# Performance work log

Measured on AMD Instinct MI355X. Metric: run time of the kernel, lower is better.

## Reference

```python
import jax, jax.numpy as jnp
import numpy as np

EMBED_DIM = 768
HEAD_DIM = 64
BATCH = 8
SEQ = 4096


def setup_inputs() -> dict:
    key = jax.random.key(0)
    k_x, k_q, k_k, k_v = jax.random.split(key, 4)
    input_ids = jax.random.normal(k_x, (BATCH, SEQ, EMBED_DIM), dtype=jnp.float32)
    # nn.Linear(embed, head, bias=False): weight shape [head, embed]; y = x @ W.T
    scale = 1.0 / np.sqrt(EMBED_DIM)
    Wq = jax.random.normal(k_q, (HEAD_DIM, EMBED_DIM), dtype=jnp.float32) * scale
    Wk = jax.random.normal(k_k, (HEAD_DIM, EMBED_DIM), dtype=jnp.float32) * scale
    Wv = jax.random.normal(k_v, (HEAD_DIM, EMBED_DIM), dtype=jnp.float32) * scale
    return {"input_ids": input_ids, "Wq": Wq, "Wk": Wk, "Wv": Wv}


def reference(input_ids, Wq, Wk, Wv):
    # Projections. NOTE: the original module (faithfully reproduced) computes
    # v with q_net, so Wv is unused in the forward math.
    q = jnp.einsum('bse,he->bsh', input_ids, Wq)  # [B,S,H]
    k = jnp.einsum('bse,he->bsh', input_ids, Wk)  # [B,S,H]
    v = jnp.einsum('bse,he->bsh', input_ids, Wq)  # bug in source: uses q_net
    seq_len = q.shape[1]
    # Non-standard scaling: divide by sqrt(seq_len), not sqrt(head_dim)
    scores = jnp.einsum('bqh,bkh->bqk', q, k) / jnp.sqrt(jnp.float32(seq_len))
    # Non-standard softmax axis: over the query axis (dim=1)
    attn_weights = jax.nn.softmax(scores, axis=1)  # [B,Sq,Sk]
    return jnp.einsum('bqk,bkh->bqh', attn_weights, v)
```

## Files before the change

### kernel.cpp

```cpp
#include <hip/hip_runtime.h>
#include <hip/hip_bf16.h>
#include <cstdint>


#define BATCH 8
#define SEQ   4096
#define EMB   768
#define HD    64
#define NROW  (BATCH*SEQ)

#define QSCALE 0.1803368801111201f
#define KSCALE 0.125f
#define CSCALE 5.545177444479562f

typedef float  f32x4  __attribute__((ext_vector_type(4)));
typedef float  f32x16 __attribute__((ext_vector_type(16)));
typedef __bf16 bf16x8 __attribute__((ext_vector_type(8)));
typedef unsigned short u16x8_t __attribute__((ext_vector_type(8)));
typedef unsigned int   u32x4_t __attribute__((ext_vector_type(4)));

__device__ __forceinline__ f32x4 mfma16(bf16x8 a, bf16x8 b, f32x4 c) {
  return __builtin_amdgcn_mfma_f32_16x16x32_bf16(a, b, c, 0, 0, 0);
}
__device__ __forceinline__ f32x16 mfma32(bf16x8 a, bf16x8 b, f32x16 c) {
  return __builtin_amdgcn_mfma_f32_32x32x16_bf16(a, b, c, 0, 0, 0);
}
__device__ __forceinline__ unsigned short f2b(float f) {
  __bf16 h = (__bf16)f;
  return __builtin_bit_cast(unsigned short, h);
}
__device__ __forceinline__ float b2f(unsigned short u) {
  unsigned int x = ((unsigned int)u) << 16;
  return __builtin_bit_cast(float, x);
}
__device__ __forceinline__ unsigned short f2h(float f) {
  _Float16 h = (_Float16)f;
  return __builtin_bit_cast(unsigned short, h);
}
__device__ __forceinline__ float h2f(unsigned short u) {
  return (float)__builtin_bit_cast(_Float16, u);
}
__device__ __forceinline__ bf16x8 ldsA(const unsigned short* p) {
  return __builtin_bit_cast(bf16x8, *(const u16x8_t*)p);
}
__device__ __forceinline__ bf16x8 ldg8(const unsigned short* p) {
  return __builtin_bit_cast(bf16x8, *(const u16x8_t*)p);
}
__device__ __forceinline__ float expf2(float x) {
  float r; asm("v_exp_f32 %0, %1" : "=v"(r) : "v"(x)); return r;
}
__device__ __forceinline__ unsigned cvtpk(float lo, float hi) {
  unsigned r; asm("v_cvt_pk_bf16_f32 %0, %1, %2" : "=v"(r) : "v"(lo), "v"(hi)); return r;
}
__device__ __forceinline__ void plane32swap(unsigned &a, unsigned &b) {
  asm volatile("v_permlane32_swap_b32 %0, %1" : "+v"(a), "+v"(b));
}
__device__ __forceinline__ void glld16(const void* g, void* l) {
  __builtin_amdgcn_global_load_lds(
      (const __attribute__((address_space(1))) void*)g,
      (__attribute__((address_space(3))) void*)l, 16, 0, 0);
}
__device__ __forceinline__ int sidx(int r, int h) {
  return r * 64 + (h ^ ((r & 7) << 3));
}

__global__ __launch_bounds__(256) void wcvt_kernel(
    const float* __restrict__ Wq, const float* __restrict__ Wk,
    unsigned short* __restrict__ Wb) {
  int ci = blockIdx.x * 256 + threadIdx.x;
  int r = ci / 96, c8 = ci % 96;
  const float* src = (r < 64 ? Wq + (size_t)r * EMB : Wk + (size_t)(r - 64) * EMB) + c8 * 8;
  float4 a = *(const float4*)src, d = *(const float4*)(src + 4);
  u16x8_t o;
  o[0]=f2b(a.x); o[1]=f2b(a.y); o[2]=f2b(a.z); o[3]=f2b(a.w);
  o[4]=f2b(d.x); o[5]=f2b(d.y); o[6]=f2b(d.z); o[7]=f2b(d.w);
  *(u16x8_t*)(Wb + (size_t)ci * 8) = o;
}

__global__ __launch_bounds__(256) void proj_kernel(
    const float* __restrict__ X, const unsigned short* __restrict__ Wb,
    unsigned short* __restrict__ Qb, unsigned short* __restrict__ Kb) {
  __shared__ unsigned short Ws[2][8192];
  const int t = threadIdx.x, lane = t & 63, w = t >> 6;
  const int c = lane & 15, g = lane >> 4;
  const int row0 = blockIdx.x * 64;
  f32x4 acc[8];
#pragma unroll
  for (int f = 0; f < 8; ++f) { acc[f][0]=0.f; acc[f][1]=0.f; acc[f][2]=0.f; acc[f][3]=0.f; }

  auto STAGE = [&](int ec, int bb) {
#pragma unroll
    for (int i = 0; i < 4; ++i) {
      int rr = w + 4 * i;
      int ci = rr * 64 + lane;
      int r = ci >> 3, cL = ci & 7;
      glld16(Wb + (size_t)r * EMB + ec * 64 + (cL ^ (r & 7)) * 8, (void*)&Ws[bb][rr * 512]);
    }
  };
  STAGE(0, 0);
  __syncthreads();
  for (int ec = 0; ec < 12; ++ec) {
    if (ec < 11) STAGE(ec + 1, (ec + 1) & 1);
    bf16x8 Af[2];
#pragma unroll
    for (int es = 0; es < 2; ++es) {
      const float* xp = X + (size_t)(row0 + 16 * w + c) * EMB + ec * 64 + es * 32 + 8 * g;
      float4 v0 = *(const float4*)xp, v1 = *(const float4*)(xp + 4);
      u16x8_t tmp;
      tmp[0]=f2b(v0.x); tmp[1]=f2b(v0.y); tmp[2]=f2b(v0.z); tmp[3]=f2b(v0.w);
      tmp[4]=f2b(v1.x); tmp[5]=f2b(v1.y); tmp[6]=f2b(v1.z); tmp[7]=f2b(v1.w);
      Af[es] = __builtin_bit_cast(bf16x8, tmp);
    }
    const unsigned short* Wt = Ws[ec & 1];
#pragma unroll
    for (int es = 0; es < 2; ++es)
#pragma unroll
      for (int f = 0; f < 8; ++f) {
        bf16x8 Bf = ldsA(&Wt[sidx(16 * f + c, es * 32 + 8 * g)]);
        acc[f] = mfma16(Af[es], Bf, acc[f]);
      }
    __syncthreads();
  }
#pragma unroll
  for (int f = 0; f < 8; ++f) {
    int n = 16 * f + c;
    float sc = (n < 64) ? QSCALE : KSCALE;
#pragma unroll
    for (int r = 0; r < 4; ++r) {
      int ROW = row0 + 16 * w + 4 * g + r;
      unsigned short bv = f2b(acc[f][r] * sc);
      if (n < 64) Qb[(size_t)ROW * 64 + n] = bv;
      else        Kb[(size_t)ROW * 64 + (n - 64)] = bv;
    }
  }
}

__global__ __launch_bounds__(256) void colsum_kernel(
    const unsigned short* __restrict__ Qb, const unsigned short* __restrict__ Kb,
    float* __restrict__ Zpart) {
  __shared__ unsigned short Qs[2][8192];
  const int t = threadIdx.x, lane = t & 63, w = t >> 6;
  const int c = lane & 31, hi = lane >> 5;
  const int fid = blockIdx.x;
  const int b = fid & 7, rem = fid >> 3;
  const int kt = rem & 15, qs = rem >> 4;
  const size_t kbase = (size_t)b * SEQ + kt * 256;
  const size_t qbase0 = (size_t)b * SEQ + qs * 1024;

  bf16x8 Kf[2][4];
#pragma unroll
  for (int j = 0; j < 2; ++j)
#pragma unroll
    for (int es = 0; es < 4; ++es)
      Kf[j][es] = __builtin_bit_cast(bf16x8,
          *(const u16x8_t*)(Kb + (kbase + 64 * w + 32 * j + c) * 64 + 16 * es + 8 * hi));

  auto STAGE = [&](int qi, int bb) {
#pragma unroll
    for (int i = 0; i < 4; ++i) {
      int rr = w + 4 * i;
      int ci = rr * 64 + lane;
      int r = ci >> 3, cL = ci & 7;
      glld16(Qb + (qbase0 + qi * 128 + r) * 64 + (cL ^ (r & 7)) * 8, (void*)&Qs[bb][rr * 512]);
    }
  };
  float csum[2] = {0.f, 0.f};
  STAGE(0, 0);
  __syncthreads();
  for (int qi = 0; qi < 8; ++qi) {
    if (qi < 7) STAGE(qi + 1, (qi + 1) & 1);
    const unsigned short* Qt = Qs[qi & 1];
#pragma unroll
    for (int sq = 0; sq < 4; ++sq) {
      bf16x8 A[4];
#pragma unroll
      for (int es = 0; es < 4; ++es)
        A[es] = ldsA(&Qt[sidx(32 * sq + c, 16 * es + 8 * hi)]);
#pragma unroll
      for (int j = 0; j < 2; ++j) {
        f32x16 sv;
#pragma unroll
        for (int i = 0; i < 16; ++i) sv[i] = 0.f;
#pragma unroll
        for (int es = 0; es < 4; ++es) sv = mfma32(A[es], Kf[j][es], sv);
#pragma unroll
        for (int i = 0; i < 16; ++i) csum[j] += expf2(sv[i]);
      }
    }
    __syncthreads();
  }
#pragma unroll
  for (int j = 0; j < 2; ++j) {
    float v = csum[j] + __shfl_xor(csum[j], 32);
    if (lane < 32)
      Zpart[(kbase + 64 * w + 32 * j + lane) * 4 + qs] = v;
  }
}

__global__ __launch_bounds__(256) void vtrans_kernel(
    const unsigned short* __restrict__ Qb, const float* __restrict__ Zpart,
    unsigned short* __restrict__ VT) {
  __shared__ unsigned short T[128 * 72];
  __shared__ float cvs[128];
  const int t = threadIdx.x;
  const int kt = blockIdx.x, b = blockIdx.y;
  const size_t kbase = (size_t)b * SEQ + kt * 128;
#pragma unroll
  for (int it = 0; it < 4; ++it) {
    int ci = t + 256 * it;
    int r = ci >> 3, ch = ci & 7;
    u16x8_t v = *(const u16x8_t*)(Qb + (kbase + r) * 64 + 8 * ch);
    *(u16x8_t*)(&T[r * 72 + 8 * (ch ^ ((r >> 3) & 7))]) = v;
  }
  if (t < 128) {
    const float* zp = Zpart + (kbase + t) * 4;
    cvs[t] = CSCALE / (zp[0] + zp[1] + zp[2] + zp[3]);
  }
  __syncthreads();
#pragma unroll
  for (int it = 0; it < 4; ++it) {
    int ci = t + 256 * it;
    int h = ci >> 4, c16 = ci & 15;
    u16x8_t o;
#pragma unroll
    for (int j = 0; j < 8; ++j) {
      int r = 8 * c16 + j;
      unsigned short raw = T[r * 72 + 8 * ((h >> 3) ^ (c16 & 7)) + (h & 7)];
      o[j] = f2b(cvs[r] * b2f(raw));
    }
    *(u16x8_t*)(VT + ((size_t)(b * 64 + h)) * SEQ + kt * 128 + 8 * c16) = o;
  }
}

template <bool F16P>
__global__ __launch_bounds__(256) void attn_kernel(
    const unsigned short* __restrict__ Qb, const unsigned short* __restrict__ Kb,
    const unsigned short* __restrict__ VT, void* __restrict__ outp, int nkt) {
  __shared__ unsigned short KV[2][8192];
  const int t = threadIdx.x, lane = t & 63, w = t >> 6;
  const int c = lane & 31, hi = lane >> 5;
  const int fid = blockIdx.x;
  const int b = fid & 7, rem = fid >> 3;
  const int qt = rem & 15, ks = rem >> 4;
  const size_t brow = (size_t)b * SEQ;
  const int q0 = qt * 256;
  const int ntiles = 2 * nkt;
  const int t0 = ks * ntiles;

  bf16x8 Qf[2][4];
#pragma unroll
  for (int j = 0; j < 2; ++j)
#pragma unroll
    for (int es = 0; es < 4; ++es)
      Qf[j][es] = ldg8(Qb + (brow + q0 + 64 * w + 32 * j + c) * 64 + 16 * es + 8 * hi);

  f32x16 acc[2][2];
#pragma unroll
  for (int j = 0; j < 2; ++j)
#pragma unroll
    for (int hb = 0; hb < 2; ++hb)
#pragma unroll
      for (int i = 0; i < 16; ++i) acc[j][hb][i] = 0.f;

  auto STAGE = [&](int tt, int bb) {
    const int k0 = (t0 + tt) * 64;
    const size_t kb0 = brow + k0;
#pragma unroll
    for (int i = 0; i < 4; ++i) {
      int rr = w + 4 * i;
      if (rr < 8) {
        int ci = rr * 64 + lane;
        int r = ci >> 3, cL = ci & 7;
        glld16(Kb + (kb0 + r) * 64 + (cL ^ (r & 7)) * 8, (void*)&KV[bb][rr * 512]);
      } else {
        int ci = (rr - 8) * 64 + lane;
        int h = ci >> 3, cL = ci & 7;
        glld16(VT + ((size_t)(b * 64 + h)) * SEQ + k0 + (cL ^ (h & 7)) * 8,
               (void*)&KV[bb][4096 + (rr - 8) * 512]);
      }
    }
  };

  auto COMPUTE = [&](int bb) {
    const unsigned short* Ks = &KV[bb][0];
    const unsigned short* Vs = &KV[bb][4096];
#pragma unroll
    for (int kb = 0; kb < 2; ++kb) {
      bf16x8 KA[4];
#pragma unroll
      for (int es = 0; es < 4; ++es)
        KA[es] = ldsA(&Ks[sidx(32 * kb + c, 16 * es + 8 * hi)]);
      bf16x8 fA[2][2];
#pragma unroll
      for (int j = 0; j < 2; ++j) {
        f32x16 sv;
#pragma unroll
        for (int i = 0; i < 16; ++i) sv[i] = 0.f;
#pragma unroll
        for (int es = 0; es < 4; ++es) sv = mfma32(KA[es], Qf[j][es], sv);
        float p[16];
#pragma unroll
        for (int i = 0; i < 16; ++i) p[i] = expf2(sv[i]);
        unsigned X0 = cvtpk(p[0], p[1]),  X1 = cvtpk(p[2], p[3]);
        unsigned Y0 = cvtpk(p[4], p[5]),  Y1 = cvtpk(p[6], p[7]);
        plane32swap(X0, Y0); plane32swap(X1, Y1);
        u32x4_t F0 = {X0, X1, Y0, Y1};
        unsigned Z0 = cvtpk(p[8], p[9]),   Z1 = cvtpk(p[10], p[11]);
        unsigned W0 = cvtpk(p[12], p[13]), W1 = cvtpk(p[14], p[15]);
        plane32swap(Z0, W0); plane32swap(Z1, W1);
        u32x4_t F1 = {Z0, Z1, W0, W1};
        fA[j][0] = __builtin_bit_cast(bf16x8, F0);
        fA[j][1] = __builtin_bit_cast(bf16x8, F1);
      }
#pragma unroll
      for (int hb = 0; hb < 2; ++hb) {
        int h = 32 * hb + c;
        int col0 = 32 * kb + 8 * hi;
        bf16x8 VB0 = ldsA(&Vs[h * 64 + (col0 ^ ((h & 7) << 3))]);
        bf16x8 VB1 = ldsA(&Vs[h * 64 + ((col0 + 16) ^ ((h & 7) << 3))]);
        acc[0][hb] = mfma32(fA[0][0], VB0, acc[0][hb]);
        acc[0][hb] = mfma32(fA[0][1], VB1, acc[0][hb]);
        acc[1][hb] = mfma32(fA[1][0], VB0, acc[1][hb]);
        acc[1][hb] = mfma32(fA[1][1], VB1, acc[1][hb]);
      }
    }
  };

  STAGE(0, 0);
  __syncthreads();
  for (int tt = 0; tt < ntiles; ++tt) {
    if (tt + 1 < ntiles) STAGE(tt + 1, (tt + 1) & 1);
    COMPUTE(tt & 1);
    __syncthreads();
  }
#pragma unroll
  for (int j = 0; j < 2; ++j)
#pragma unroll
    for (int hb = 0; hb < 2; ++hb)
#pragma unroll
      for (int r = 0; r < 16; ++r) {
        int qrow = (r & 3) + 8 * (r >> 2) + 4 * hi;
        size_t idx = (brow + q0 + 64 * w + 32 * j + qrow) * 64 + 32 * hb + c;
        if (F16P) {
          unsigned short* op = (unsigned short*)outp + (size_t)ks * NROW * 64;
          op[idx] = f2h(acc[j][hb][r]);
        } else {
          ((float*)outp)[idx] = acc[j][hb][r];
        }
      }
}

__global__ __launch_bounds__(256) void osum_kernel(
    const unsigned short* __restrict__ P, float* __restrict__ O) {
  const size_t PS = (size_t)NROW * 64;
  size_t i = ((size_t)blockIdx.x * 256 + threadIdx.x) * 8;
  u16x8_t a = *(const u16x8_t*)(P + i);
  u16x8_t b = *(const u16x8_t*)(P + PS + i);
  u16x8_t c = *(const u16x8_t*)(P + 2 * PS + i);
  u16x8_t d = *(const u16x8_t*)(P + 3 * PS + i);
  float o[8];
#pragma unroll
  for (int j = 0; j < 8; ++j)
    o[j] = (h2f(a[j]) + h2f(b[j])) + (h2f(c[j]) + h2f(d[j]));
  float4 o0 = {o[0], o[1], o[2], o[3]}, o1 = {o[4], o[5], o[6], o[7]};
  *(float4*)(O + i) = o0;
  *(float4*)(O + i + 4) = o1;
}

extern "C" void kernel_launch(void* const* d_in, const int* in_sizes, int n_in,
                              void* d_out, int out_size, void* d_ws, size_t ws_size,
                              hipStream_t stream) {
  const float* X  = (const float*)d_in[0];
  const float* Wq = (const float*)d_in[1];
  const float* Wk = (const float*)d_in[2];
  float* Out = (float*)d_out;

  unsigned char* wsb = (unsigned char*)d_ws;
  const size_t QB_OFF = 0;
  const size_t KB_OFF = 4194304;
  const size_t WB_OFF = 8388608;
  const size_t Z_OFF  = 8585216;
  const size_t VT_OFF = 9240576;
  const size_t OP_OFF = 13434880;
  const size_t TOTAL_SPLIT = OP_OFF + (size_t)4 * NROW * 64 * 2;

  unsigned short* Qb = (unsigned short*)(wsb + QB_OFF);
  unsigned short* Kb = (unsigned short*)(wsb + KB_OFF);
  unsigned short* Wb = (unsigned short*)(wsb + WB_OFF);
  float* Zpart       = (float*)(wsb + Z_OFF);
  unsigned short* VT = (unsigned short*)(wsb + VT_OFF);
  unsigned short* OpH = (unsigned short*)(wsb + OP_OFF);

  const bool split = (ws_size >= TOTAL_SPLIT);

  hipLaunchKernelGGL(wcvt_kernel, dim3(48), dim3(256), 0, stream, Wq, Wk, Wb);
  hipLaunchKernelGGL(proj_kernel, dim3(NROW / 64), dim3(256), 0, stream, X, Wb, Qb, Kb);
  hipLaunchKernelGGL(colsum_kernel, dim3(512), dim3(256), 0, stream, Qb, Kb, Zpart);
  hipLaunchKernelGGL(vtrans_kernel, dim3(32, 8), dim3(256), 0, stream, Qb, Zpart, VT);
  if (split) {
    hipLaunchKernelGGL(attn_kernel<true>, dim3(512), dim3(256), 0, stream,
                       Qb, Kb, VT, (void*)OpH, 8);
    hipLaunchKernelGGL(osum_kernel, dim3(1024), dim3(256), 0, stream, OpH, Out);
  } else {
    hipLaunchKernelGGL(attn_kernel<false>, dim3(128), dim3(256), 0, stream,
                       Qb, Kb, VT, (void*)Out, 32);
  }
}
```

Before: 104.3 us.

## Triple-buffer LDS staging with partial vmcnt waits and MFMA priority hints

The colsum and attention kernels move from double to triple buffering of their Q and KV tiles in LDS, prefetching two tiles ahead. Each full __syncthreads is replaced by an s_waitcnt vmcnt(4) plus a raw barrier, so the load for the next-next tile can stay in flight across the barrier. MFMA sections are also wrapped in s_setprio to favour the matrix issue. The cost is 50% more LDS per block, which may lower occupancy, and correctness now depends on the hand-counted outstanding loads per STAGE.

```diff
diff --git a/kernel.cpp b/kernel.cpp
--- a/kernel.cpp
+++ b/kernel.cpp
@@ -59,6 +59,16 @@
   __builtin_amdgcn_global_load_lds(
       (const __attribute__((address_space(1))) void*)g,
       (__attribute__((address_space(3))) void*)l, 16, 0, 0);
+}
+__device__ __forceinline__ void vmwait4() {
+  asm volatile("s_waitcnt vmcnt(4)" ::: "memory");
+}
+__device__ __forceinline__ void vmwait0() {
+  asm volatile("s_waitcnt vmcnt(0)" ::: "memory");
+}
+__device__ __forceinline__ void barrier_raw() {
+  __builtin_amdgcn_s_barrier();
+  __builtin_amdgcn_sched_barrier(0);
 }
 __device__ __forceinline__ int sidx(int r, int h) {
   return r * 64 + (h ^ ((r & 7) << 3));
@@ -138,7 +148,7 @@
 __global__ __launch_bounds__(256) void colsum_kernel(
     const unsigned short* __restrict__ Qb, const unsigned short* __restrict__ Kb,
     float* __restrict__ Zpart) {
-  __shared__ unsigned short Qs[2][8192];
+  __shared__ unsigned short Qs[3][8192];
   const int t = threadIdx.x, lane = t & 63, w = t >> 6;
   const int c = lane & 31, hi = lane >> 5;
   const int fid = blockIdx.x;
@@ -166,10 +176,12 @@
   };
   float csum[2] = {0.f, 0.f};
   STAGE(0, 0);
-  __syncthreads();
+  STAGE(1, 1);
+  vmwait4();
+  barrier_raw();
   for (int qi = 0; qi < 8; ++qi) {
-    if (qi < 7) STAGE(qi + 1, (qi + 1) & 1);
-    const unsigned short* Qt = Qs[qi & 1];
+    if (qi + 2 < 8) STAGE(qi + 2, (qi + 2) % 3);
+    const unsigned short* Qt = Qs[qi % 3];
 #pragma unroll
     for (int sq = 0; sq < 4; ++sq) {
       bf16x8 A[4];
@@ -181,13 +193,17 @@
         f32x16 sv;
 #pragma unroll
         for (int i = 0; i < 16; ++i) sv[i] = 0.f;
+        __builtin_amdgcn_s_setprio(1);
 #pragma unroll
         for (int es = 0; es < 4; ++es) sv = mfma32(A[es], Kf[j][es], sv);
+        __builtin_amdgcn_s_setprio(0);
 #pragma unroll
         for (int i = 0; i < 16; ++i) csum[j] += expf2(sv[i]);
       }
     }
-    __syncthreads();
+    if (qi + 2 < 8)      vmwait4();
+    else if (qi + 1 < 8) vmwait0();
+    if (qi + 1 < 8)      barrier_raw();
   }
 #pragma unroll
   for (int j = 0; j < 2; ++j) {
@@ -236,7 +252,7 @@
 __global__ __launch_bounds__(256) void attn_kernel(
     const unsigned short* __restrict__ Qb, const unsigned short* __restrict__ Kb,
     const unsigned short* __restrict__ VT, void* __restrict__ outp, int nkt) {
-  __shared__ unsigned short KV[2][8192];
+  __shared__ unsigned short KV[3][8192];
   const int t = threadIdx.x, lane = t & 63, w = t >> 6;
   const int c = lane & 31, hi = lane >> 5;
   const int fid = blockIdx.x;
@@ -296,8 +312,10 @@
         f32x16 sv;
 #pragma unroll
         for (int i = 0; i < 16; ++i) sv[i] = 0.f;
+        __builtin_amdgcn_s_setprio(1);
 #pragma unroll
         for (int es = 0; es < 4; ++es) sv = mfma32(KA[es], Qf[j][es], sv);
+        __builtin_amdgcn_s_setprio(0);
         float p[16];
 #pragma unroll
         for (int i = 0; i < 16; ++i) p[i] = expf2(sv[i]);
@@ -312,6 +330,7 @@
         fA[j][0] = __builtin_bit_cast(bf16x8, F0);
         fA[j][1] = __builtin_bit_cast(bf16x8, F1);
       }
+      __builtin_amdgcn_s_setprio(1);
 #pragma unroll
       for (int hb = 0; hb < 2; ++hb) {
         int h = 32 * hb + c;
@@ -323,15 +342,20 @@
         acc[1][hb] = mfma32(fA[1][0], VB0, acc[1][hb]);
         acc[1][hb] = mfma32(fA[1][1], VB1, acc[1][hb]);
       }
+      __builtin_amdgcn_s_setprio(0);
     }
   };
 
   STAGE(0, 0);
-  __syncthreads();
+  STAGE(1, 1);
+  vmwait4();
+  barrier_raw();
   for (int tt = 0; tt < ntiles; ++tt) {
-    if (tt + 1 < ntiles) STAGE(tt + 1, (tt + 1) & 1);
-    COMPUTE(tt & 1);
-    __syncthreads();
+    if (tt + 2 < ntiles) STAGE(tt + 2, (tt + 2) % 3);
+    COMPUTE(tt % 3);
+    if (tt + 2 < ntiles)      vmwait4();
+    else if (tt + 1 < ntiles) vmwait0();
+    if (tt + 1 < ntiles)      barrier_raw();
   }
 #pragma unroll
   for (int j = 0; j < 2; ++j)
```

Result: no change. 106.0 us (+1.6%).
